# Optimization experiments

Hardware: AMD Instinct MI355X
Metric: run time of the kernel (lower is better)

Reference implementation:

```python
import jax, jax.numpy as jnp
import numpy as np

B, T, H, W_SP, C_IN = 8, 16, 64, 64, 32
F = 64  # output_channels


def _conv(x, w):
    # x: (B,H,W,Cin), w: (kh,kw,Cin,Cout), 'same' padding, stride 1
    return jax.lax.conv_general_dilated(
        x, w, window_strides=(1, 1), padding='SAME',
        dimension_numbers=('NHWC', 'HWIO', 'NHWC'))


def setup_inputs() -> dict:
    key = jax.random.key(0)
    k1, k2, k3 = jax.random.split(key, 3)
    x = jax.random.normal(k1, (B, T, H, W_SP, C_IN), dtype=jnp.float32)
    # Keras ConvLSTM2D kernels: gates stacked [i, f, c, o] along last axis
    W = jax.random.normal(k2, (3, 3, C_IN, 4 * F), dtype=jnp.float32) * 0.05
    U = jax.random.normal(k3, (3, 3, F, 4 * F), dtype=jnp.float32) * 0.05
    b = jnp.zeros((4 * F,), dtype=jnp.float32)
    return {"x": x, "W": W, "U": U, "b": b}


def reference(x, W, U, b):
    # ConvLSTM2D: activation='relu', recurrent_activation='hard_sigmoid',
    # return_sequences=False -> final hidden state (B,H,W,F)
    rec_act = jax.nn.hard_sigmoid  # relu6(x+3)/6
    act = jax.nn.relu

    h0 = jnp.zeros((x.shape[0], x.shape[2], x.shape[3], F), dtype=x.dtype)
    c0 = jnp.zeros_like(h0)

    def step(carry, x_t):
        h, c = carry
        z = _conv(x_t, W) + _conv(h, U) + b  # (B,H,W,4F)
        zi, zf, zc, zo = jnp.split(z, 4, axis=-1)
        i = rec_act(zi)
        f = rec_act(zf)
        o = rec_act(zo)
        c_new = f * c + i * act(zc)
        h_new = o * act(c_new)
        return (h_new, c_new), None

    xs = jnp.transpose(x, (1, 0, 2, 3, 4))  # (T,B,H,W,Cin)
    (h_final, _), _ = jax.lax.scan(step, (h0, c0), xs)
    return h_final
```

## Files before the change

kernel.cpp:

```cpp
#include <hip/hip_runtime.h>


#define TSTEPS 16

typedef short bf16x8 __attribute__((ext_vector_type(8)));
typedef float f32x4 __attribute__((ext_vector_type(4)));
typedef unsigned int __attribute__((address_space(1))) gu32;
typedef unsigned int __attribute__((address_space(3))) lu32;

__device__ __forceinline__ float hsig(float x) {
    return fminf(fmaxf((x + 3.0f) * (1.0f / 6.0f), 0.0f), 1.0f);
}

__device__ __forceinline__ unsigned short f2bf(float f) {
    union { float f; unsigned int u; } v; v.f = f;
    unsigned int r = v.u + 0x7fffu + ((v.u >> 16) & 1u);
    return (unsigned short)(r >> 16);
}

__global__ __launch_bounds__(256)
void prepack_w(const float* __restrict__ Wg, const float* __restrict__ Ug,
               unsigned short* __restrict__ out)
{
    int idx = blockIdx.x * 256 + threadIdx.x;
    if (idx >= 27648) return;
    int lane = idx & 63;
    int nt   = (idx >> 6) & 15;
    int s    = idx >> 10;
    int col = lane & 15, quad = lane >> 4;
    int n = nt * 16 + col;
    int k0 = quad * 8;
    const float* src;
    if (s < 9) {
        src = Wg + ((size_t)s * 32 + k0) * 256 + n;
    } else {
        int ss = s - 9; int tap = ss >> 1; int half = ss & 1;
        src = Ug + ((size_t)tap * 64 + half * 32 + k0) * 256 + n;
    }
    unsigned short tmp[8];
    #pragma unroll
    for (int j = 0; j < 8; ++j) tmp[j] = f2bf(src[(size_t)j * 256]);
    *(uint4*)(out + (size_t)idx * 8) = *(uint4*)tmp;
}

template<int NS>
__global__ __launch_bounds__(256)
__attribute__((amdgpu_waves_per_eu(2, 2)))
void convlstm_step(const float* __restrict__ x,
                   const unsigned short* __restrict__ wpk,
                   const float* __restrict__ bias,
                   const unsigned short* __restrict__ h_in,
                   float* __restrict__ c_st,
                   unsigned short* __restrict__ h_out,
                   int t, int is_last)
{
    constexpr bool HP = (NS == 27);
    constexpr int  P  = 3;

    __shared__ __align__(16) unsigned short xs_s[100 * 40];
    __shared__ __align__(16) unsigned short hs_s[HP ? 100 * 72 : 8];
    __shared__ __align__(16) unsigned short bring[P * 16 * 512];

    const int tid = threadIdx.x;
    const int gx0 = blockIdx.x * 8;
    const int gy0 = blockIdx.y * 8;
    const int b   = blockIdx.z;

    {
        const float* xt = x + (((size_t)b * TSTEPS + t) * (size_t)(64 * 64 * 32));
        #pragma unroll 4
        for (int idx = tid; idx < 100 * 8; idx += 256) {
            int pix = idx >> 3, q = idx & 7;
            int iy = pix / 10, ix = pix - iy * 10;
            int gy = gy0 + iy - 1, gx = gx0 + ix - 1;
            unsigned short o[4] = {0, 0, 0, 0};
            if ((unsigned)gy < 64u && (unsigned)gx < 64u) {
                float4 v = *(const float4*)(xt + ((size_t)(gy * 64 + gx) * 32) + q * 4);
                o[0] = f2bf(v.x); o[1] = f2bf(v.y); o[2] = f2bf(v.z); o[3] = f2bf(v.w);
            }
            *(ushort4*)(xs_s + pix * 40 + q * 4) = *(ushort4*)o;
        }
    }
    if constexpr (HP) {
        const unsigned short* hb = h_in + ((size_t)b * (64 * 64 * 64));
        #pragma unroll 4
        for (int idx = tid; idx < 100 * 8; idx += 256) {
            int pix = idx >> 3, q = idx & 7;
            int iy = pix / 10, ix = pix - iy * 10;
            int gy = gy0 + iy - 1, gx = gx0 + ix - 1;
            uint4 v = make_uint4(0u, 0u, 0u, 0u);
            if ((unsigned)gy < 64u && (unsigned)gx < 64u)
                v = *(const uint4*)(hb + ((size_t)(gy * 64 + gx) * 64) + q * 8);
            *(uint4*)(hs_s + pix * 72 + q * 8) = v;
        }
    }
    __syncthreads();

    const int lane = tid & 63;
    const int w    = tid >> 6;
    const int quad = lane >> 4;
    const int m    = lane & 15;
    const int col  = m;
    const int ch   = w * 16 + col;

    int xb[4], hb_[4];
    #pragma unroll
    for (int mt = 0; mt < 4; ++mt) {
        int p = mt * 16 + m;
        int py = p >> 3, px = p & 7;
        xb[mt]  = (py * 10 + px) * 40 + quad * 8;
        hb_[mt] = (py * 10 + px) * 72 + quad * 8;
    }

    auto issueDMA = [&](int s) {
        int slot = s % P;
        #pragma unroll
        for (int g = 0; g < 4; ++g) {
            int nt = w + 4 * g;
            const unsigned short* gp = wpk + ((size_t)(s * 16 + nt) * 64 + lane) * 8;
            unsigned short* lp = bring + ((size_t)slot * 16 + nt) * 512;
            __builtin_amdgcn_global_load_lds((const gu32*)gp, (lu32*)lp, 16, 0, 0);
        }
    };

    f32x4 acc[4][4];
    #pragma unroll
    for (int g = 0; g < 4; ++g) {
        float bv = bias[g * 64 + ch];
        f32x4 bi = (f32x4){bv, bv, bv, bv};
        #pragma unroll
        for (int mt = 0; mt < 4; ++mt) acc[mt][g] = bi;
    }

    issueDMA(0);
    issueDMA(1);
    issueDMA(2);

    #pragma unroll
    for (int s = 0; s < NS; ++s) {
        if (s + 2 < NS)      __builtin_amdgcn_s_waitcnt(0xF78);
        else if (s + 1 < NS) __builtin_amdgcn_s_waitcnt(0xF74);
        else                 __builtin_amdgcn_s_waitcnt(0xF70);

        const int slot = s % P;
        bf16x8 bfr[4];
        #pragma unroll
        for (int g = 0; g < 4; ++g)
            bfr[g] = *(const bf16x8*)(bring + ((size_t)slot * 16 + (w + 4 * g)) * 512 + lane * 8);

        bf16x8 a[4];
        if (s < 9) {
            int taplin = (s / 3) * 10 + (s % 3);
            #pragma unroll
            for (int mt = 0; mt < 4; ++mt)
                a[mt] = *(const bf16x8*)(xs_s + xb[mt] + taplin * 40);
        } else {
            int ss = s - 9, tap = ss >> 1, half = ss & 1;
            int taplin = (tap / 3) * 10 + (tap % 3);
            #pragma unroll
            for (int mt = 0; mt < 4; ++mt)
                a[mt] = *(const bf16x8*)(hs_s + hb_[mt] + taplin * 72 + half * 32);
        }

        #pragma unroll
        for (int g = 0; g < 4; ++g)
            #pragma unroll
            for (int mt = 0; mt < 4; ++mt)
                acc[mt][g] = __builtin_amdgcn_mfma_f32_16x16x32_bf16(a[mt], bfr[g], acc[mt][g], 0, 0, 0);

        if (s + P < NS) issueDMA(s + P);
    }

    #pragma unroll
    for (int mt = 0; mt < 4; ++mt) {
        #pragma unroll
        for (int r = 0; r < 4; ++r) {
            int p = mt * 16 + quad * 4 + r;
            int py = p >> 3, px = p & 7;
            size_t gidx = (((size_t)b * 64 + (gy0 + py)) * 64 + (gx0 + px)) * 64 + ch;
            float zi = acc[mt][0][r];
            float zf = acc[mt][1][r];
            float zc = acc[mt][2][r];
            float zo = acc[mt][3][r];
            float c_prev = HP ? c_st[gidx] : 0.0f;
            float cn = hsig(zf) * c_prev + hsig(zi) * fmaxf(zc, 0.0f);
            float hn = hsig(zo) * fmaxf(cn, 0.0f);
            if (is_last) {
                c_st[gidx] = hn;
            } else {
                c_st[gidx] = cn;
                h_out[gidx] = f2bf(hn);
            }
        }
    }
}

extern "C" void kernel_launch(void* const* d_in, const int* in_sizes, int n_in,
                              void* d_out, int out_size, void* d_ws, size_t ws_size,
                              hipStream_t stream) {
    const float* x  = (const float*)d_in[0];
    const float* Wg = (const float*)d_in[1];
    const float* Ug = (const float*)d_in[2];
    const float* bs = (const float*)d_in[3];

    unsigned short* wpk = (unsigned short*)d_ws;
    unsigned short* h0  = (unsigned short*)((char*)d_ws + 27 * 16 * 64 * 8 * 2);
    unsigned short* h1  = h0 + (size_t)8 * 64 * 64 * 64;
    float* cS = (float*)d_out;

    prepack_w<<<108, 256, 0, stream>>>(Wg, Ug, wpk);

    dim3 grid(8, 8, 8);
    dim3 block(256);
    for (int t = 0; t < TSTEPS; ++t) {
        const unsigned short* hin = (t == 0) ? h0 : ((t & 1) ? h0 : h1);
        unsigned short* hout = (t & 1) ? h1 : h0;
        if (t == 0) {
            convlstm_step<9><<<grid, block, 0, stream>>>(x, wpk, bs, hin, cS, hout, t, 0);
        } else {
            convlstm_step<27><<<grid, block, 0, stream>>>(x, wpk, bs, hin, cS, hout,
                                                          t, (t == TSTEPS - 1) ? 1 : 0);
        }
    }
}
```

Baseline: 443.0 us.

## Split output channels across two blocks and gather gates through LDS

Each tile is now split across two blocks by output-channel half, which doubles the grid and halves the per-wave accumulators and weight traffic. Each wave computes one gate for 32 channels, so the four gates are exchanged through a reused shared-memory buffer before the elementwise LSTM update. This is meant to raise occupancy (waves_per_eu 4, fewer registers, less LDS) and parallelism. The cost is that both blocks redundantly load and convert the same input and hidden halo tiles, and the prefetch ring shrinks from triple to double buffering.

New measurement: 464.3 us. 4.8% more time.

```diff
diff --git a/kernel.cpp b/kernel.cpp
--- a/kernel.cpp
+++ b/kernel.cpp
@@ -45,7 +45,7 @@
 
 template<int NS>
 __global__ __launch_bounds__(256)
-__attribute__((amdgpu_waves_per_eu(2, 2)))
+__attribute__((amdgpu_waves_per_eu(4)))
 void convlstm_step(const float* __restrict__ x,
                    const unsigned short* __restrict__ wpk,
                    const float* __restrict__ bias,
@@ -55,16 +55,37 @@
                    int t, int is_last)
 {
     constexpr bool HP = (NS == 27);
-    constexpr int  P  = 3;
-
-    __shared__ __align__(16) unsigned short xs_s[100 * 40];
-    __shared__ __align__(16) unsigned short hs_s[HP ? 100 * 72 : 8];
-    __shared__ __align__(16) unsigned short bring[P * 16 * 512];
+
+    __shared__ __align__(16) unsigned char smem[38784];
+    unsigned short* xs_s  = (unsigned short*)smem;
+    unsigned short* hs_s  = (unsigned short*)(smem + 8000);
+    unsigned short* bring = (unsigned short*)(smem + 22400);
+    float*          zbuf  = (float*)smem;
 
     const int tid = threadIdx.x;
     const int gx0 = blockIdx.x * 8;
     const int gy0 = blockIdx.y * 8;
-    const int b   = blockIdx.z;
+    const int b   = blockIdx.z >> 1;
+    const int nh  = blockIdx.z & 1;
+
+    const int lane = tid & 63;
+    const int w    = tid >> 6;
+    const int quad = lane >> 4;
+    const int m    = lane & 15;
+
+    auto issueDMA = [&](int s) {
+        int slot = s & 1;
+        #pragma unroll
+        for (int g = 0; g < 2; ++g) {
+            int ntg = w * 4 + nh * 2 + g;
+            const unsigned short* gp = wpk + ((size_t)(s * 16 + ntg) * 64 + lane) * 8;
+            unsigned short* lp = bring + ((size_t)(slot * 8 + w * 2 + g)) * 512;
+            __builtin_amdgcn_global_load_lds((const gu32*)gp, (lu32*)lp, 16, 0, 0);
+        }
+    };
+
+    issueDMA(0);
+    issueDMA(1);
 
     {
         const float* xt = x + (((size_t)b * TSTEPS + t) * (size_t)(64 * 64 * 32));
@@ -96,13 +117,6 @@
     }
     __syncthreads();
 
-    const int lane = tid & 63;
-    const int w    = tid >> 6;
-    const int quad = lane >> 4;
-    const int m    = lane & 15;
-    const int col  = m;
-    const int ch   = w * 16 + col;
-
     int xb[4], hb_[4];
     #pragma unroll
     for (int mt = 0; mt < 4; ++mt) {
@@ -112,41 +126,25 @@
         hb_[mt] = (py * 10 + px) * 72 + quad * 8;
     }
 
-    auto issueDMA = [&](int s) {
-        int slot = s % P;
-        #pragma unroll
-        for (int g = 0; g < 4; ++g) {
-            int nt = w + 4 * g;
-            const unsigned short* gp = wpk + ((size_t)(s * 16 + nt) * 64 + lane) * 8;
-            unsigned short* lp = bring + ((size_t)slot * 16 + nt) * 512;
-            __builtin_amdgcn_global_load_lds((const gu32*)gp, (lu32*)lp, 16, 0, 0);
-        }
-    };
-
-    f32x4 acc[4][4];
-    #pragma unroll
-    for (int g = 0; g < 4; ++g) {
-        float bv = bias[g * 64 + ch];
+    f32x4 acc[4][2];
+    #pragma unroll
+    for (int g = 0; g < 2; ++g) {
+        float bv = bias[w * 64 + nh * 32 + g * 16 + m];
         f32x4 bi = (f32x4){bv, bv, bv, bv};
         #pragma unroll
         for (int mt = 0; mt < 4; ++mt) acc[mt][g] = bi;
     }
 
-    issueDMA(0);
-    issueDMA(1);
-    issueDMA(2);
-
     #pragma unroll
     for (int s = 0; s < NS; ++s) {
-        if (s + 2 < NS)      __builtin_amdgcn_s_waitcnt(0xF78);
-        else if (s + 1 < NS) __builtin_amdgcn_s_waitcnt(0xF74);
-        else                 __builtin_amdgcn_s_waitcnt(0xF70);
-
-        const int slot = s % P;
-        bf16x8 bfr[4];
-        #pragma unroll
-        for (int g = 0; g < 4; ++g)
-            bfr[g] = *(const bf16x8*)(bring + ((size_t)slot * 16 + (w + 4 * g)) * 512 + lane * 8);
+        if (s + 1 < NS) __builtin_amdgcn_s_waitcnt(0xF72);
+        else            __builtin_amdgcn_s_waitcnt(0xF70);
+
+        const int slot = s & 1;
+        bf16x8 bfr[2];
+        #pragma unroll
+        for (int g = 0; g < 2; ++g)
+            bfr[g] = *(const bf16x8*)(bring + ((size_t)(slot * 8 + w * 2 + g)) * 512 + lane * 8);
 
         bf16x8 a[4];
         if (s < 9) {
@@ -163,28 +161,42 @@
         }
 
         #pragma unroll
-        for (int g = 0; g < 4; ++g)
+        for (int g = 0; g < 2; ++g)
             #pragma unroll
             for (int mt = 0; mt < 4; ++mt)
                 acc[mt][g] = __builtin_amdgcn_mfma_f32_16x16x32_bf16(a[mt], bfr[g], acc[mt][g], 0, 0, 0);
 
-        if (s + P < NS) issueDMA(s + P);
-    }
-
-    #pragma unroll
-    for (int mt = 0; mt < 4; ++mt) {
-        #pragma unroll
-        for (int r = 0; r < 4; ++r) {
-            int p = mt * 16 + quad * 4 + r;
-            int py = p >> 3, px = p & 7;
-            size_t gidx = (((size_t)b * 64 + (gy0 + py)) * 64 + (gx0 + px)) * 64 + ch;
-            float zi = acc[mt][0][r];
-            float zf = acc[mt][1][r];
-            float zc = acc[mt][2][r];
-            float zo = acc[mt][3][r];
+        if (s + 2 < NS) {
+            __builtin_amdgcn_sched_barrier(0);
+            issueDMA(s + 2);
+        }
+    }
+
+    __syncthreads();
+
+    #pragma unroll
+    for (int mt = 0; mt < 4; ++mt)
+        #pragma unroll
+        for (int g = 0; g < 2; ++g)
+            #pragma unroll
+            for (int r = 0; r < 4; ++r) {
+                int px = mt * 16 + quad * 4 + r;
+                zbuf[((px * 32) + g * 16 + m) * 4 + w] = acc[mt][g][r];
+            }
+    __syncthreads();
+
+    {
+        const int chbase = nh * 32;
+        #pragma unroll
+        for (int j = 0; j < 8; ++j) {
+            int c = j * 256 + tid;
+            int fch = c & 31, px = c >> 5;
+            int py = px >> 3, pxx = px & 7;
+            float4 z = *(const float4*)(zbuf + (size_t)c * 4);
+            size_t gidx = (((size_t)b * 64 + (gy0 + py)) * 64 + (gx0 + pxx)) * 64 + chbase + fch;
             float c_prev = HP ? c_st[gidx] : 0.0f;
-            float cn = hsig(zf) * c_prev + hsig(zi) * fmaxf(zc, 0.0f);
-            float hn = hsig(zo) * fmaxf(cn, 0.0f);
+            float cn = hsig(z.y) * c_prev + hsig(z.x) * fmaxf(z.z, 0.0f);
+            float hn = hsig(z.w) * fmaxf(cn, 0.0f);
             if (is_last) {
                 c_st[gidx] = hn;
             } else {
@@ -210,7 +222,7 @@
 
     prepack_w<<<108, 256, 0, stream>>>(Wg, Ug, wpk);
 
-    dim3 grid(8, 8, 8);
+    dim3 grid(8, 8, 16);
     dim3 block(256);
     for (int t = 0; t < TSTEPS; ++t) {
         const unsigned short* hin = (t == 0) ? h0 : ((t & 1) ? h0 : h1);
```
